# Kernel tuning notes

Hardware: AMD Instinct MI355X
Metric: run time of the kernel (lower is better)

The kernel has to match this reference:

```python
import jax, jax.numpy as jnp
import numpy as np

N, E, L, D = 4, 64, 512, 768


def setup_inputs() -> dict:
    key = jax.random.key(0)
    k1, k2, k3, k4 = jax.random.split(key, 4)
    doc_state = jax.random.normal(k1, (N, L, D), dtype=jnp.float32)
    # 0/1 entity membership mask, float as in the torch module's multiply
    entity_mapping = jax.random.randint(k2, (N, E, L), 0, 2).astype(jnp.float32)
    # lens consistent with the mask; clamp to >=1 to avoid divide-by-zero
    entity_lens = jnp.maximum(entity_mapping.sum(axis=-1), 1.0)
    W = jax.random.normal(k3, (D, 2 * D), dtype=jnp.float32) * 0.02  # torch Linear weight [out, in]
    b = jnp.zeros((D,), dtype=jnp.float32)
    return {"doc_state": doc_state, "entity_mapping": entity_mapping,
            "entity_lens": entity_lens, "W": W, "b": b}


def reference(doc_state, entity_mapping, entity_lens, W, b):
    # entity_states: N x E x L x d (the large broadcast intermediate)
    entity_states = entity_mapping[:, :, :, None] * doc_state[:, None, :, :]
    max_pooled = jnp.max(entity_states, axis=2)                      # N x E x d
    mean_pooled = jnp.sum(entity_states, axis=2) / entity_lens[:, :, None]  # N x E x d
    output = jnp.concatenate([max_pooled, mean_pooled], axis=2)      # N x E x 2d
    return jnp.einsum('nek,dk->ned', output, W) + b                  # N x E x d
```

## Files before the change

### kernel.cpp

```cpp
#include <hip/hip_runtime.h>
#include <hip/hip_bf16.h>
#include <math.h>

#define PN 4
#define PE 64
#define PL 512
#define PD 768
#define PK2 (2 * PD)
#define PM (PN * PE)

#define EG 4
#define DCW 64
#define NDC (PD / DCW)
#define NPOOLB (PN * (PE / EG) * NDC)
#define NCVT 288

using bf16x8 = __attribute__((ext_vector_type(8))) short;
using f32x4  = __attribute__((ext_vector_type(4))) float;

static __device__ __forceinline__ unsigned short f2bf(float x) {
    unsigned int u = __float_as_uint(x);
    unsigned int r = (u + 0x7FFFu + ((u >> 16) & 1u)) >> 16;
    return (unsigned short)r;
}

__global__ __launch_bounds__(512) void pool_v5(
    const float* __restrict__ doc,
    const float* __restrict__ map,
    const float* __restrict__ lens,
    const float* __restrict__ W,
    unsigned short* __restrict__ Pb,
    unsigned short* __restrict__ Wb)
{
    const int bid = blockIdx.x;
    const int tid = threadIdx.x;

    if (bid >= NPOOLB) {
        const size_t i = ((size_t)(bid - NPOOLB) * 512 + tid) * 8;
        const float4 a = *reinterpret_cast<const float4*>(W + i);
        const float4 c = *reinterpret_cast<const float4*>(W + i + 4);
        union { unsigned short s[8]; uint4 v; } r;
        r.s[0] = f2bf(a.x); r.s[1] = f2bf(a.y); r.s[2] = f2bf(a.z); r.s[3] = f2bf(a.w);
        r.s[4] = f2bf(c.x); r.s[5] = f2bf(c.y); r.s[6] = f2bf(c.z); r.s[7] = f2bf(c.w);
        *reinterpret_cast<uint4*>(Wb + i) = r.v;
        return;
    }

    __shared__ float lmax[8][EG][64];
    __shared__ float lsum[8][EG][64];

    const int dc   = bid % NDC;
    const int rest = bid / NDC;
    const int eg   = rest & 15;
    const int n    = rest >> 4;
    const int e0   = eg * EG;
    const int d0   = dc * DCW;
    const int w    = tid >> 6;
    const int lane = tid & 63;

    unsigned long long mk[EG];
    #pragma unroll
    for (int e = 0; e < EG; ++e) {
        const float m = map[((size_t)n * PE + e0 + e) * PL + w * 64 + lane];
        mk[e] = __ballot(m != 0.0f);
    }

    const float* docp = doc + ((size_t)n * PL + w * 64) * PD + d0 + lane;

    float mx[EG], sm[EG];
    #pragma unroll
    for (int e = 0; e < EG; ++e) { mx[e] = -INFINITY; sm[e] = 0.f; }

    #pragma unroll 16
    for (int l = 0; l < 64; ++l) {
        const float v = docp[(size_t)l * PD];
        #pragma unroll
        for (int e = 0; e < EG; ++e) {
            const float mval = ((mk[e] >> l) & 1ull) ? 1.0f : 0.0f;
            const float cand = mval * v;
            sm[e] += cand;
            mx[e] = fmaxf(mx[e], cand);
        }
    }

    #pragma unroll
    for (int e = 0; e < EG; ++e) {
        lmax[w][e][lane] = mx[e];
        lsum[w][e][lane] = sm[e];
    }
    __syncthreads();

    const int slot = tid & 255;
    const int e  = slot >> 6;
    const int ln = slot & 63;
    const int ne = n * PE + e0 + e;
    const int d  = d0 + ln;
    if (tid < 256) {
        float m = lmax[0][e][ln];
        #pragma unroll
        for (int ww = 1; ww < 8; ++ww) m = fmaxf(m, lmax[ww][e][ln]);
        Pb[(size_t)ne * PK2 + d] = f2bf(m);
    } else {
        float s = lsum[0][e][ln];
        #pragma unroll
        for (int ww = 1; ww < 8; ++ww) s += lsum[ww][e][ln];
        Pb[(size_t)ne * PK2 + PD + d] = f2bf(s * (1.0f / lens[ne]));
    }
}

__global__ __launch_bounds__(128) void gemm_ks2(
    const unsigned short* __restrict__ Pb,
    const unsigned short* __restrict__ Wb,
    const float* __restrict__ b,
    float* __restrict__ out)
{
    __shared__ f32x4 red[64];

    const int w    = threadIdx.x >> 6;
    const int lane = threadIdx.x & 63;
    const int tile = blockIdx.x;
    const int rt = tile & 15;
    const int ct = tile >> 4;
    const int r0 = rt * 16, d0 = ct * 16;

    const int fr = lane & 15;
    const int kg = lane >> 4;
    const int kb = w * (PK2 / 2);

    const unsigned short* pA = Pb + (size_t)(r0 + fr) * PK2 + kb + kg * 8;
    const unsigned short* pB = Wb + (size_t)(d0 + fr) * PK2 + kb + kg * 8;

    f32x4 acc0 = {0.f, 0.f, 0.f, 0.f};
    f32x4 acc1 = {0.f, 0.f, 0.f, 0.f};
    #pragma unroll
    for (int k0 = 0; k0 < PK2 / 2; k0 += 64) {
        const bf16x8 a0 = *reinterpret_cast<const bf16x8*>(pA + k0);
        const bf16x8 b0 = *reinterpret_cast<const bf16x8*>(pB + k0);
        acc0 = __builtin_amdgcn_mfma_f32_16x16x32_bf16(a0, b0, acc0, 0, 0, 0);
        const bf16x8 a1 = *reinterpret_cast<const bf16x8*>(pA + k0 + 32);
        const bf16x8 b1 = *reinterpret_cast<const bf16x8*>(pB + k0 + 32);
        acc1 = __builtin_amdgcn_mfma_f32_16x16x32_bf16(a1, b1, acc1, 0, 0, 0);
    }
    f32x4 acc = acc0 + acc1;

    if (w == 1) red[lane] = acc;
    __syncthreads();
    if (w == 0) {
        acc += red[lane];
        const int c = d0 + fr;
        const float bias = b[c];
        #pragma unroll
        for (int j = 0; j < 4; ++j)
            out[(size_t)(r0 + kg * 4 + j) * PD + c] = acc[j] + bias;
    }
}

__global__ __launch_bounds__(256) void fused_kernel(
    const float* __restrict__ doc, const float* __restrict__ map,
    const float* __restrict__ lens, const float* __restrict__ W,
    const float* __restrict__ b, float* __restrict__ out)
{
    __shared__ float Prow[PK2];
    const int ne = blockIdx.x, n = ne >> 6, t = threadIdx.x;
    const float* docn = doc + (size_t)n * PL * PD;
    const float* mrow = map + (size_t)ne * PL;
    float mx0=-INFINITY, mx1=-INFINITY, mx2=-INFINITY, s0=0.f, s1=0.f, s2=0.f;
    bool has_zero = false;
    for (int l = 0; l < PL; ++l) {
        const float m = mrow[l];
        if (m != 0.0f) {
            const float* dr = docn + (size_t)l * PD;
            const float a = dr[t], c = dr[t+256], e = dr[t+512];
            mx0=fmaxf(mx0,a); s0+=a; mx1=fmaxf(mx1,c); s1+=c; mx2=fmaxf(mx2,e); s2+=e;
        } else has_zero = true;
    }
    if (has_zero) { mx0=fmaxf(mx0,0.f); mx1=fmaxf(mx1,0.f); mx2=fmaxf(mx2,0.f); }
    const float invlen = 1.0f / lens[ne];
    Prow[t]=mx0; Prow[t+256]=mx1; Prow[t+512]=mx2;
    Prow[PD+t]=s0*invlen; Prow[PD+t+256]=s1*invlen; Prow[PD+t+512]=s2*invlen;
    __syncthreads();
    #pragma unroll
    for (int i = 0; i < 3; ++i) {
        const int d = t + i*256;
        const float* wrow = W + (size_t)d * PK2;
        float acc = 0.f;
        for (int k = 0; k < PK2; k += 4) {
            const float4 w = *reinterpret_cast<const float4*>(&wrow[k]);
            acc += Prow[k]*w.x + Prow[k+1]*w.y + Prow[k+2]*w.z + Prow[k+3]*w.w;
        }
        out[(size_t)ne * PD + d] = acc + b[d];
    }
}

extern "C" void kernel_launch(void* const* d_in, const int* in_sizes, int n_in,
                              void* d_out, int out_size, void* d_ws, size_t ws_size,
                              hipStream_t stream) {
    const float* doc  = (const float*)d_in[0];
    const float* map  = (const float*)d_in[1];
    const float* lens = (const float*)d_in[2];
    const float* W    = (const float*)d_in[3];
    const float* b    = (const float*)d_in[4];
    float* out = (float*)d_out;

    const size_t pb_bytes = (size_t)PM * PK2 * sizeof(unsigned short);
    const size_t wb_bytes = (size_t)PD * PK2 * sizeof(unsigned short);
    const size_t need     = pb_bytes + wb_bytes;

    if (ws_size >= need) {
        unsigned short* Pb = (unsigned short*)d_ws;
        unsigned short* Wb = (unsigned short*)((char*)d_ws + pb_bytes);
        pool_v5<<<dim3(NPOOLB + NCVT), dim3(512), 0, stream>>>(
            doc, map, lens, W, Pb, Wb);
        gemm_ks2<<<dim3((PM / 16) * (PD / 16)), dim3(128), 0, stream>>>(Pb, Wb, b, out);
    } else {
        fused_kernel<<<dim3(PM), dim3(256), 0, stream>>>(doc, map, lens, W, b, out);
    }
}
```

Before: 30.47 us.

## Pool 16 entities per block and remap GEMM tiles per XCD

The pooling kernel now handles 16 entities per block instead of 4, so each doc_state element loaded is reused across four times as many entities, and the number of pooling blocks drops from 768 to 192. The reduction epilogue is rewritten so every thread finalizes two adjacent features for both max and mean and writes them as packed 32-bit stores. The GEMM block index is remapped so that blocks landing on the same XCD share a contiguous range of W column tiles, aiming at better L2 locality. The risks are higher register pressure from 32 accumulators per thread and fewer pooling blocks to spread across the CUs.

```diff
diff --git a/kernel.cpp b/kernel.cpp
--- a/kernel.cpp
+++ b/kernel.cpp
@@ -9,11 +9,12 @@
 #define PK2 (2 * PD)
 #define PM (PN * PE)
 
-#define EG 4
+#define EG 16
 #define DCW 64
 #define NDC (PD / DCW)
 #define NPOOLB (PN * (PE / EG) * NDC)
 #define NCVT 288
+#define NXCD 8
 
 using bf16x8 = __attribute__((ext_vector_type(8))) short;
 using f32x4  = __attribute__((ext_vector_type(4))) float;
@@ -24,7 +25,7 @@
     return (unsigned short)r;
 }
 
-__global__ __launch_bounds__(512) void pool_v5(
+__global__ __launch_bounds__(512) void pool_v7(
     const float* __restrict__ doc,
     const float* __restrict__ map,
     const float* __restrict__ lens,
@@ -51,8 +52,8 @@
 
     const int dc   = bid % NDC;
     const int rest = bid / NDC;
-    const int eg   = rest & 15;
-    const int n    = rest >> 4;
+    const int eg   = rest & 3;
+    const int n    = rest >> 2;
     const int e0   = eg * EG;
     const int d0   = dc * DCW;
     const int w    = tid >> 6;
@@ -71,7 +72,7 @@
     #pragma unroll
     for (int e = 0; e < EG; ++e) { mx[e] = -INFINITY; sm[e] = 0.f; }
 
-    #pragma unroll 16
+    #pragma unroll 4
     for (int l = 0; l < 64; ++l) {
         const float v = docp[(size_t)l * PD];
         #pragma unroll
@@ -90,25 +91,28 @@
     }
     __syncthreads();
 
-    const int slot = tid & 255;
-    const int e  = slot >> 6;
-    const int ln = slot & 63;
+    const int e  = tid >> 5;
+    const int dd = (tid & 31) << 1;
     const int ne = n * PE + e0 + e;
-    const int d  = d0 + ln;
-    if (tid < 256) {
-        float m = lmax[0][e][ln];
-        #pragma unroll
-        for (int ww = 1; ww < 8; ++ww) m = fmaxf(m, lmax[ww][e][ln]);
-        Pb[(size_t)ne * PK2 + d] = f2bf(m);
-    } else {
-        float s = lsum[0][e][ln];
-        #pragma unroll
-        for (int ww = 1; ww < 8; ++ww) s += lsum[ww][e][ln];
-        Pb[(size_t)ne * PK2 + PD + d] = f2bf(s * (1.0f / lens[ne]));
-    }
-}
-
-__global__ __launch_bounds__(128) void gemm_ks2(
+    const int d  = d0 + dd;
+
+    float m0 = lmax[0][e][dd], m1 = lmax[0][e][dd + 1];
+    float s0 = lsum[0][e][dd], s1 = lsum[0][e][dd + 1];
+    #pragma unroll
+    for (int ww = 1; ww < 8; ++ww) {
+        m0 = fmaxf(m0, lmax[ww][e][dd]);
+        m1 = fmaxf(m1, lmax[ww][e][dd + 1]);
+        s0 += lsum[ww][e][dd];
+        s1 += lsum[ww][e][dd + 1];
+    }
+    const float inv = 1.0f / lens[ne];
+    const unsigned int pkm = (unsigned int)f2bf(m0) | ((unsigned int)f2bf(m1) << 16);
+    const unsigned int pks = (unsigned int)f2bf(s0 * inv) | ((unsigned int)f2bf(s1 * inv) << 16);
+    *reinterpret_cast<unsigned int*>(Pb + (size_t)ne * PK2 + d)      = pkm;
+    *reinterpret_cast<unsigned int*>(Pb + (size_t)ne * PK2 + PD + d) = pks;
+}
+
+__global__ __launch_bounds__(128) void gemm_ks2x(
     const unsigned short* __restrict__ Pb,
     const unsigned short* __restrict__ Wb,
     const float* __restrict__ b,
@@ -118,9 +122,11 @@
 
     const int w    = threadIdx.x >> 6;
     const int lane = threadIdx.x & 63;
-    const int tile = blockIdx.x;
-    const int rt = tile & 15;
-    const int ct = tile >> 4;
+    const int bid  = blockIdx.x;
+    const int xcd  = bid & (NXCD - 1);
+    const int idx  = bid >> 3;
+    const int ct = xcd * 6 + (idx >> 4);
+    const int rt = idx & 15;
     const int r0 = rt * 16, d0 = ct * 16;
 
     const int fr = lane & 15;
@@ -209,9 +215,9 @@
     if (ws_size >= need) {
         unsigned short* Pb = (unsigned short*)d_ws;
         unsigned short* Wb = (unsigned short*)((char*)d_ws + pb_bytes);
-        pool_v5<<<dim3(NPOOLB + NCVT), dim3(512), 0, stream>>>(
+        pool_v7<<<dim3(NPOOLB + NCVT), dim3(512), 0, stream>>>(
             doc, map, lens, W, Pb, Wb);
-        gemm_ks2<<<dim3((PM / 16) * (PD / 16)), dim3(128), 0, stream>>>(Pb, Wb, b, out);
+        gemm_ks2x<<<dim3((PM / 16) * (PD / 16)), dim3(128), 0, stream>>>(Pb, Wb, b, out);
     } else {
         fused_kernel<<<dim3(PM), dim3(256), 0, stream>>>(doc, map, lens, W, b, out);
     }
```

After: 35.00 us. 1.15x slower.
